# Performance work log

Measured on AMD Instinct MI355X. Metric: run time of the kernel, lower is better.

The kernel has to match this reference:

```python
import jax, jax.numpy as jnp
import numpy as np
import math

N_HEADS = 16
D_EMBED = 1024
D_CROSS = 768
FF_DIM = 4096
D_HEAD = D_EMBED // N_HEADS
LN_EPS = 1e-5


def layer_norm(h, g, b):
    mu = jnp.mean(h, axis=-1, keepdims=True)
    var = jnp.var(h, axis=-1, keepdims=True)
    return (h - mu) * jax.lax.rsqrt(var + LN_EPS) * g + b


def mha(q, k, v):
    # q: [B,Sq,D], k/v: [B,Skv,D] -> split heads, attend, merge
    B, Sq, _ = q.shape
    Skv = k.shape[1]
    qh = q.reshape(B, Sq, N_HEADS, D_HEAD).transpose(0, 2, 1, 3)
    kh = k.reshape(B, Skv, N_HEADS, D_HEAD).transpose(0, 2, 1, 3)
    vh = v.reshape(B, Skv, N_HEADS, D_HEAD).transpose(0, 2, 1, 3)
    scores = jnp.einsum('bhqd,bhkd->bhqk', qh, kh) / math.sqrt(D_HEAD)
    attn = jax.nn.softmax(scores, axis=-1)
    out = jnp.einsum('bhqk,bhkd->bhqd', attn, vh)
    return out.transpose(0, 2, 1, 3).reshape(B, Sq, D_EMBED)


def setup_inputs() -> dict:
    key = jax.random.key(0)
    ks = jax.random.split(key, 24)
    s = 0.02
    inp = {
        'x': jax.random.normal(ks[0], (4, 1024, D_EMBED), jnp.float32),
        'y': jax.random.normal(ks[1], (4, 77, D_CROSS), jnp.float32),
        # self-attention in_proj (d_embed -> 3*d_embed) and out_proj
        'w_qkv': jax.random.normal(ks[2], (D_EMBED, 3 * D_EMBED), jnp.float32) * s,
        'b_qkv': jnp.zeros((3 * D_EMBED,), jnp.float32),
        'w_so': jax.random.normal(ks[3], (D_EMBED, D_EMBED), jnp.float32) * s,
        'b_so': jnp.zeros((D_EMBED,), jnp.float32),
        # cross-attention projections
        'w_q': jax.random.normal(ks[4], (D_EMBED, D_EMBED), jnp.float32) * s,
        'b_q': jnp.zeros((D_EMBED,), jnp.float32),
        'w_k': jax.random.normal(ks[5], (D_CROSS, D_EMBED), jnp.float32) * s,
        'b_k': jnp.zeros((D_EMBED,), jnp.float32),
        'w_v': jax.random.normal(ks[6], (D_CROSS, D_EMBED), jnp.float32) * s,
        'b_v': jnp.zeros((D_EMBED,), jnp.float32),
        'w_co': jax.random.normal(ks[7], (D_EMBED, D_EMBED), jnp.float32) * s,
        'b_co': jnp.zeros((D_EMBED,), jnp.float32),
        # 3-layer FFN
        'w1': jax.random.normal(ks[8], (D_EMBED, FF_DIM), jnp.float32) * s,
        'b1': jnp.zeros((FF_DIM,), jnp.float32),
        'w2': jax.random.normal(ks[9], (FF_DIM, FF_DIM), jnp.float32) * s,
        'b2': jnp.zeros((FF_DIM,), jnp.float32),
        'w3': jax.random.normal(ks[10], (FF_DIM, D_EMBED), jnp.float32) * s,
        'b3': jnp.zeros((D_EMBED,), jnp.float32),
        # single shared LayerNorm (used 3 times, as in the torch module)
        'ln_g': jnp.ones((D_EMBED,), jnp.float32),
        'ln_b': jnp.zeros((D_EMBED,), jnp.float32),
    }
    return inp


def reference(x, y, w_qkv, b_qkv, w_so, b_so, w_q, b_q, w_k, b_k, w_v, b_v,
              w_co, b_co, w1, b1, w2, b2, w3, b3, ln_g, ln_b):
    # --- self attention (no causal mask) ---
    qkv = x @ w_qkv + b_qkv
    q, k, v = jnp.split(qkv, 3, axis=-1)
    sa = mha(q, k, v) @ w_so + b_so
    x = layer_norm(x + sa, ln_g, ln_b)
    # --- cross attention ---
    qc = x @ w_q + b_q
    kc = y @ w_k + b_k
    vc = y @ w_v + b_v
    ca = mha(qc, kc, vc) @ w_co + b_co
    x = layer_norm(x + ca, ln_g, ln_b)
    # --- 3-layer FFN with ReLU ---
    h = jax.nn.relu(x @ w1 + b1)
    h = jax.nn.relu(h @ w2 + b2)
    ff = h @ w3 + b3
    x = layer_norm(x + ff, ln_g, ln_b)
    return x
```

## Files before the change

kernel.cpp:

```cpp
#include <hip/hip_runtime.h>
#include <hip/hip_bf16.h>
#include <math.h>

typedef short v8s __attribute__((ext_vector_type(8)));
typedef float v4f __attribute__((ext_vector_type(4)));

__device__ __forceinline__ unsigned short f2bf(float f) {
  union { float f; unsigned u; } a; a.f = f;
  unsigned u = a.u + 0x7fffu + ((a.u >> 16) & 1u);
  return (unsigned short)(u >> 16);
}

__device__ __forceinline__ void gld_lds16(const unsigned short* g, unsigned short* l) {
  __builtin_amdgcn_global_load_lds(
      (const __attribute__((address_space(1))) void*)g,
      (__attribute__((address_space(3))) void*)l,
      16, 0, 0);
}

__global__ void cvt_f32_bf16(const float* __restrict__ in,
                             unsigned short* __restrict__ out, int n4) {
  int i = blockIdx.x * blockDim.x + threadIdx.x;
  if (i >= n4) return;
  float4 v = reinterpret_cast<const float4*>(in)[i];
  ushort4 o;
  o.x = f2bf(v.x); o.y = f2bf(v.y); o.z = f2bf(v.z); o.w = f2bf(v.w);
  reinterpret_cast<ushort4*>(out)[i] = o;
}

__global__ void cvt_transpose(const float* __restrict__ in,
                              unsigned short* __restrict__ out, int K, int N) {
  __shared__ float t[32][33];
  int bx = blockIdx.x, by = blockIdx.y;
  int tx = threadIdx.x, ty = threadIdx.y;
#pragma unroll
  for (int i = 0; i < 4; i++) {
    int k = by * 32 + ty + i * 8;
    t[ty + i * 8][tx] = in[(size_t)k * N + bx * 32 + tx];
  }
  __syncthreads();
#pragma unroll
  for (int i = 0; i < 4; i++) {
    int n = bx * 32 + ty + i * 8;
    out[(size_t)n * K + by * 32 + tx] = f2bf(t[tx][ty + i * 8]);
  }
}

template<bool RELU, bool OUTF, bool OUTB>
__global__ __launch_bounds__(256)
void gemm_bf16(const unsigned short* __restrict__ A,
               const unsigned short* __restrict__ BT,
               const float* __restrict__ bias,
               float* __restrict__ Cf, unsigned short* __restrict__ Cb,
               int M, int N, int K) {
  __shared__ __align__(16) unsigned short lA[128 * 64];
  __shared__ __align__(16) unsigned short lB[128 * 64];
  int tid  = threadIdx.x;
  int lane = tid & 63;
  int wave = tid >> 6;
  int wr = (wave >> 1) * 64;
  int wc = (wave & 1) * 64;
  int quad = lane >> 4;
  int l15  = lane & 15;
  int m0 = blockIdx.y * 128;
  int n0 = blockIdx.x * 128;

  int srow   = tid >> 3;
  int schunk = (tid & 7) ^ (srow & 7);
  const unsigned short* gA = A  + (size_t)(m0 + srow) * K + schunk * 8;
  const unsigned short* gB = BT + (size_t)(n0 + srow) * K + schunk * 8;
  unsigned short* ldsA = lA + wave * 512;
  unsigned short* ldsB = lB + wave * 512;
  const size_t rowblk = (size_t)32 * K;

  const v4f vzero = {0.f, 0.f, 0.f, 0.f};
  v4f acc[4][4];
#pragma unroll
  for (int i = 0; i < 4; i++)
#pragma unroll
    for (int j = 0; j < 4; j++) acc[i][j] = vzero;

  for (int k0 = 0; k0 < K; k0 += 64) {
#pragma unroll
    for (int i = 0; i < 4; i++) {
      gld_lds16(gA + k0 + i * rowblk, ldsA + i * 2048);
      gld_lds16(gB + k0 + i * rowblk, ldsB + i * 2048);
    }
    __syncthreads();
#pragma unroll
    for (int s = 0; s < 2; s++) {
      v8s aF[4], bF[4];
#pragma unroll
      for (int i = 0; i < 4; i++)
        aF[i] = *(const v8s*)&lA[(wr + i * 16 + l15) * 64 + (((s * 4 + quad) ^ (l15 & 7)) * 8)];
#pragma unroll
      for (int j = 0; j < 4; j++)
        bF[j] = *(const v8s*)&lB[(wc + j * 16 + l15) * 64 + (((s * 4 + quad) ^ (l15 & 7)) * 8)];
#pragma unroll
      for (int i = 0; i < 4; i++)
#pragma unroll
        for (int j = 0; j < 4; j++)
          acc[i][j] = __builtin_amdgcn_mfma_f32_16x16x32_bf16(aF[i], bF[j], acc[i][j], 0, 0, 0);
    }
    __syncthreads();
  }

#pragma unroll
  for (int j = 0; j < 4; j++) {
    int col = n0 + wc + j * 16 + l15;
    float bv = bias ? bias[col] : 0.f;
#pragma unroll
    for (int i = 0; i < 4; i++) {
#pragma unroll
      for (int r = 0; r < 4; r++) {
        int row = m0 + wr + i * 16 + quad * 4 + r;
        if (row < M) {
          float v = acc[i][j][r] + bv;
          if (RELU) v = fmaxf(v, 0.f);
          if (OUTF) Cf[(size_t)row * N + col] = v;
          if (OUTB) Cb[(size_t)row * N + col] = f2bf(v);
        }
      }
    }
  }
}

__global__ __launch_bounds__(256)
void attn_kernel(const unsigned short* __restrict__ Q,
                 const unsigned short* __restrict__ K,
                 const unsigned short* __restrict__ V,
                 unsigned short* __restrict__ O,
                 int q_rowstride, int kv_rowstride, int o_rowstride,
                 int q_batch_rows, int kv_batch_rows, int Skv, float scale) {
  __shared__ __align__(16) unsigned short lK[64][72];
  __shared__ __align__(16) unsigned short lV[64][72];
  __shared__ __align__(16) unsigned short lP[4][16][72];
  int tid  = threadIdx.x;
  int lane = tid & 63;
  int wave = tid >> 6;
  int quad = lane >> 4;
  int l15  = lane & 15;
  int qt = blockIdx.x, h = blockIdx.y, b = blockIdx.z;

  const unsigned short* Qb = Q + (size_t)b * q_batch_rows * q_rowstride + h * 64;
  const unsigned short* Kb = K + (size_t)b * kv_batch_rows * kv_rowstride + h * 64;
  const unsigned short* Vb = V + (size_t)b * kv_batch_rows * kv_rowstride + h * 64;

  v8s qf0, qf1;
  {
    const unsigned short* qr = Qb + (size_t)(qt * 64 + wave * 16 + l15) * q_rowstride + quad * 8;
    qf0 = *(const v8s*)(qr);
    qf1 = *(const v8s*)(qr + 32);
  }

  const v4f vzero = {0.f, 0.f, 0.f, 0.f};
  v4f o_acc[4];
#pragma unroll
  for (int t = 0; t < 4; t++) o_acc[t] = vzero;
  float m_r[4], l_r[4];
#pragma unroll
  for (int r = 0; r < 4; r++) { m_r[r] = -1e30f; l_r[r] = 0.f; }

  int sr = tid >> 2;
  int sc = (tid & 3) * 16;

  int nch = (Skv + 63) >> 6;
  for (int ch = 0; ch < nch; ch++) {
    int base = ch * 64;
    int gr = base + sr;
    v8s k0v = {}, k1v = {}, v0v = {}, v1v = {};
    if (gr < Skv) {
      const unsigned short* kp = Kb + (size_t)gr * kv_rowstride + sc;
      const unsigned short* vp = Vb + (size_t)gr * kv_rowstride + sc;
      k0v = *(const v8s*)kp;  k1v = *(const v8s*)(kp + 8);
      v0v = *(const v8s*)vp;  v1v = *(const v8s*)(vp + 8);
    }
    __syncthreads();
    *(v8s*)&lK[sr][sc]     = k0v;
    *(v8s*)&lK[sr][sc + 8] = k1v;
#pragma unroll
    for (int e = 0; e < 8; e++) {
      lV[sc + e][sr]     = (unsigned short)v0v[e];
      lV[sc + 8 + e][sr] = (unsigned short)v1v[e];
    }
    __syncthreads();

    float s[4][4];
#pragma unroll
    for (int t = 0; t < 4; t++) {
      v8s kf0 = *(const v8s*)&lK[t * 16 + l15][quad * 8];
      v8s kf1 = *(const v8s*)&lK[t * 16 + l15][32 + quad * 8];
      v4f sacc = vzero;
      sacc = __builtin_amdgcn_mfma_f32_16x16x32_bf16(qf0, kf0, sacc, 0, 0, 0);
      sacc = __builtin_amdgcn_mfma_f32_16x16x32_bf16(qf1, kf1, sacc, 0, 0, 0);
      int kvpos = base + t * 16 + l15;
      bool ok = kvpos < Skv;
#pragma unroll
      for (int r = 0; r < 4; r++) s[t][r] = ok ? sacc[r] * scale : -1e30f;
    }

#pragma unroll
    for (int r = 0; r < 4; r++) {
      float mx = fmaxf(fmaxf(s[0][r], s[1][r]), fmaxf(s[2][r], s[3][r]));
#pragma unroll
      for (int d = 1; d < 16; d <<= 1) mx = fmaxf(mx, __shfl_xor(mx, d));
      float mnew = fmaxf(m_r[r], mx);
      float alpha = __expf(m_r[r] - mnew);
      float sm = 0.f;
#pragma unroll
      for (int t = 0; t < 4; t++) { s[t][r] = __expf(s[t][r] - mnew); sm += s[t][r]; }
#pragma unroll
      for (int d = 1; d < 16; d <<= 1) sm += __shfl_xor(sm, d);
      l_r[r] = l_r[r] * alpha + sm;
      m_r[r] = mnew;
#pragma unroll
      for (int t = 0; t < 4; t++) o_acc[t][r] *= alpha;
    }

#pragma unroll
    for (int t = 0; t < 4; t++)
#pragma unroll
      for (int r = 0; r < 4; r++)
        lP[wave][quad * 4 + r][t * 16 + l15] = f2bf(s[t][r]);
    __syncthreads();
    v8s pf0 = *(const v8s*)&lP[wave][l15][quad * 8];
    v8s pf1 = *(const v8s*)&lP[wave][l15][32 + quad * 8];
#pragma unroll
    for (int t = 0; t < 4; t++) {
      v8s vf0 = *(const v8s*)&lV[t * 16 + l15][quad * 8];
      v8s vf1 = *(const v8s*)&lV[t * 16 + l15][32 + quad * 8];
      o_acc[t] = __builtin_amdgcn_mfma_f32_16x16x32_bf16(pf0, vf0, o_acc[t], 0, 0, 0);
      o_acc[t] = __builtin_amdgcn_mfma_f32_16x16x32_bf16(pf1, vf1, o_acc[t], 0, 0, 0);
    }
  }

  int orow0 = b * q_batch_rows + qt * 64 + wave * 16;
#pragma unroll
  for (int t = 0; t < 4; t++) {
#pragma unroll
    for (int r = 0; r < 4; r++) {
      float v = o_acc[t][r] / l_r[r];
      O[(size_t)(orow0 + quad * 4 + r) * o_rowstride + h * 64 + t * 16 + l15] = f2bf(v);
    }
  }
}

__global__ __launch_bounds__(256)
void ln_kernel(const float* base, const float* __restrict__ delta,
               const float* __restrict__ g, const float* __restrict__ bb,
               float* outf, unsigned short* __restrict__ outb) {
  __shared__ float red[8];
  int row = blockIdx.x;
  int tid = threadIdx.x;
  float4 vb = ((const float4*)(base  + (size_t)row * 1024))[tid];
  float4 vd = ((const float4*)(delta + (size_t)row * 1024))[tid];
  float v0 = vb.x + vd.x, v1 = vb.y + vd.y, v2 = vb.z + vd.z, v3 = vb.w + vd.w;
  float s = v0 + v1 + v2 + v3;
  float q = v0 * v0 + v1 * v1 + v2 * v2 + v3 * v3;
#pragma unroll
  for (int d = 1; d < 64; d <<= 1) { s += __shfl_xor(s, d); q += __shfl_xor(q, d); }
  int wave = tid >> 6, lane = tid & 63;
  if (lane == 0) { red[wave] = s; red[4 + wave] = q; }
  __syncthreads();
  s = red[0] + red[1] + red[2] + red[3];
  q = red[4] + red[5] + red[6] + red[7];
  float mean = s * (1.f / 1024.f);
  float var  = q * (1.f / 1024.f) - mean * mean;
  float rstd = rsqrtf(var + 1e-5f);
  float4 gg  = ((const float4*)g)[tid];
  float4 bv  = ((const float4*)bb)[tid];
  float o0 = (v0 - mean) * rstd * gg.x + bv.x;
  float o1 = (v1 - mean) * rstd * gg.y + bv.y;
  float o2 = (v2 - mean) * rstd * gg.z + bv.z;
  float o3 = (v3 - mean) * rstd * gg.w + bv.w;
  if (outf) {
    float4 o; o.x = o0; o.y = o1; o.z = o2; o.w = o3;
    ((float4*)(outf + (size_t)row * 1024))[tid] = o;
  }
  if (outb) {
    ushort4 u; u.x = f2bf(o0); u.y = f2bf(o1); u.z = f2bf(o2); u.w = f2bf(o3);
    ((ushort4*)(outb + (size_t)row * 1024))[tid] = u;
  }
}

extern "C" void kernel_launch(void* const* d_in, const int* in_sizes, int n_in,
                              void* d_out, int out_size, void* d_ws, size_t ws_size,
                              hipStream_t stream) {
  const float* x     = (const float*)d_in[0];
  const float* y     = (const float*)d_in[1];
  const float* w_qkv = (const float*)d_in[2];
  const float* b_qkv = (const float*)d_in[3];
  const float* w_so  = (const float*)d_in[4];
  const float* b_so  = (const float*)d_in[5];
  const float* w_q   = (const float*)d_in[6];
  const float* b_q   = (const float*)d_in[7];
  const float* w_k   = (const float*)d_in[8];
  const float* b_k   = (const float*)d_in[9];
  const float* w_v   = (const float*)d_in[10];
  const float* b_v   = (const float*)d_in[11];
  const float* w_co  = (const float*)d_in[12];
  const float* b_co  = (const float*)d_in[13];
  const float* w1    = (const float*)d_in[14];
  const float* b1    = (const float*)d_in[15];
  const float* w2    = (const float*)d_in[16];
  const float* b2    = (const float*)d_in[17];
  const float* w3    = (const float*)d_in[18];
  const float* b3    = (const float*)d_in[19];
  const float* ln_g  = (const float*)d_in[20];
  const float* ln_b  = (const float*)d_in[21];

  char* ws = (char*)d_ws;
  auto US = [&](size_t off) { return (unsigned short*)(ws + off); };
  auto FP = [&](size_t off) { return (float*)(ws + off); };

  constexpr size_t o_wqkv = 0;
  constexpr size_t o_wso  = o_wqkv + 3072ull * 1024 * 2;
  constexpr size_t o_wq   = o_wso  + 1024ull * 1024 * 2;
  constexpr size_t o_wk   = o_wq   + 1024ull * 1024 * 2;
  constexpr size_t o_wv   = o_wk   + 1024ull * 768 * 2;
  constexpr size_t o_wco  = o_wv   + 1024ull * 768 * 2;
  constexpr size_t o_w1   = o_wco  + 1024ull * 1024 * 2;
  constexpr size_t o_w2   = o_w1   + 4096ull * 1024 * 2;
  constexpr size_t o_w3   = o_w2   + 4096ull * 4096 * 2;
  constexpr size_t o_xf   = o_w3   + 1024ull * 4096 * 2;
  constexpr size_t o_xbf  = o_xf   + 4096ull * 1024 * 4;
  constexpr size_t o_ybf  = o_xbf  + 4096ull * 1024 * 2;
  constexpr size_t o_dlt  = o_ybf  + 308ull * 768 * 2;
  constexpr size_t o_R1   = o_dlt  + 4096ull * 1024 * 4;
  constexpr size_t o_attn = o_R1   + 4096ull * 3072 * 2;
  constexpr size_t o_R2   = o_attn + 4096ull * 1024 * 2;
  constexpr size_t o_qc = o_R1;
  constexpr size_t o_kc = o_R1 + 4096ull * 1024 * 2;
  constexpr size_t o_vc = o_kc + 308ull * 1024 * 2;
  constexpr size_t o_h1 = o_R1;
  constexpr size_t o_h2 = o_R2;

  dim3 tb(32, 8);
  cvt_transpose<<<dim3(96, 32),  tb, 0, stream>>>(w_qkv, US(o_wqkv), 1024, 3072);
  cvt_transpose<<<dim3(32, 32),  tb, 0, stream>>>(w_so,  US(o_wso),  1024, 1024);
  cvt_transpose<<<dim3(32, 32),  tb, 0, stream>>>(w_q,   US(o_wq),   1024, 1024);
  cvt_transpose<<<dim3(32, 24),  tb, 0, stream>>>(w_k,   US(o_wk),   768,  1024);
  cvt_transpose<<<dim3(32, 24),  tb, 0, stream>>>(w_v,   US(o_wv),   768,  1024);
  cvt_transpose<<<dim3(32, 32),  tb, 0, stream>>>(w_co,  US(o_wco),  1024, 1024);
  cvt_transpose<<<dim3(128, 32), tb, 0, stream>>>(w1,    US(o_w1),   1024, 4096);
  cvt_transpose<<<dim3(128, 128),tb, 0, stream>>>(w2,    US(o_w2),   4096, 4096);
  cvt_transpose<<<dim3(32, 128), tb, 0, stream>>>(w3,    US(o_w3),   4096, 1024);

  cvt_f32_bf16<<<4096, 256, 0, stream>>>(x, US(o_xbf), 4096 * 1024 / 4);
  cvt_f32_bf16<<<231, 256, 0, stream>>>(y, US(o_ybf), 4 * 77 * 768 / 4);

  gemm_bf16<false, false, true><<<dim3(24, 32), 256, 0, stream>>>(
      US(o_xbf), US(o_wqkv), b_qkv, nullptr, US(o_R1), 4096, 3072, 1024);
  attn_kernel<<<dim3(16, 16, 4), 256, 0, stream>>>(
      US(o_R1), US(o_R1) + 1024, US(o_R1) + 2048, US(o_attn),
      3072, 3072, 1024, 1024, 1024, 1024, 0.125f);
  gemm_bf16<false, true, false><<<dim3(8, 32), 256, 0, stream>>>(
      US(o_attn), US(o_wso), b_so, FP(o_dlt), nullptr, 4096, 1024, 1024);
  ln_kernel<<<4096, 256, 0, stream>>>(x, FP(o_dlt), ln_g, ln_b, FP(o_xf), US(o_xbf));

  gemm_bf16<false, false, true><<<dim3(8, 32), 256, 0, stream>>>(
      US(o_xbf), US(o_wq), b_q, nullptr, US(o_qc), 4096, 1024, 1024);
  gemm_bf16<false, false, true><<<dim3(8, 3), 256, 0, stream>>>(
      US(o_ybf), US(o_wk), b_k, nullptr, US(o_kc), 308, 1024, 768);
  gemm_bf16<false, false, true><<<dim3(8, 3), 256, 0, stream>>>(
      US(o_ybf), US(o_wv), b_v, nullptr, US(o_vc), 308, 1024, 768);
  attn_kernel<<<dim3(16, 16, 4), 256, 0, stream>>>(
      US(o_qc), US(o_kc), US(o_vc), US(o_attn),
      1024, 1024, 1024, 1024, 77, 77, 0.125f);
  gemm_bf16<false, true, false><<<dim3(8, 32), 256, 0, stream>>>(
      US(o_attn), US(o_wco), b_co, FP(o_dlt), nullptr, 4096, 1024, 1024);
  ln_kernel<<<4096, 256, 0, stream>>>(FP(o_xf), FP(o_dlt), ln_g, ln_b, FP(o_xf), US(o_xbf));

  gemm_bf16<true, false, true><<<dim3(32, 32), 256, 0, stream>>>(
      US(o_xbf), US(o_w1), b1, nullptr, US(o_h1), 4096, 4096, 1024);
  gemm_bf16<true, false, true><<<dim3(32, 32), 256, 0, stream>>>(
      US(o_h1), US(o_w2), b2, nullptr, US(o_h2), 4096, 4096, 4096);
  gemm_bf16<false, true, false><<<dim3(8, 32), 256, 0, stream>>>(
      US(o_h2), US(o_w3), b3, FP(o_dlt), nullptr, 4096, 1024, 4096);
  ln_kernel<<<4096, 256, 0, stream>>>(FP(o_xf), FP(o_dlt), ln_g, ln_b, (float*)d_out, nullptr);
}
```

Before: 837.5 us.

## Split-K the N=1024 projections, pre-transpose V, drop redundant attention barrier

The output projections and the final FFN GEMM (N=1024) now run as a two-way split-K over blockIdx.z. Each half writes its own fp32 partial buffer, and LayerNorm sums both deltas. This doubles the block count on GEMMs that otherwise fill only 256 tiles. A separate transpose_v kernel pre-lays V as [d][kv], so the attention kernel can do vector LDS stores instead of scalar transposed writes. A per-wave __syncthreads before reading P is also removed. The cost is an extra fp32 partial write and read, plus an extra small transpose kernel per attention.

Result: faster. 811.5 us (-3.1%).

```diff
diff --git a/kernel.cpp b/kernel.cpp
--- a/kernel.cpp
+++ b/kernel.cpp
@@ -3,6 +3,7 @@
 #include <math.h>
 
 typedef short v8s __attribute__((ext_vector_type(8)));
+typedef short v4s __attribute__((ext_vector_type(4)));
 typedef float v4f __attribute__((ext_vector_type(4)));
 
 __device__ __forceinline__ unsigned short f2bf(float f) {
@@ -46,13 +47,41 @@
   }
 }
 
+__global__ __launch_bounds__(256)
+void transpose_v(const unsigned short* __restrict__ V,
+                 unsigned short* __restrict__ Vt,
+                 int rowstride, int batch_rows, int Skv, int kvpad) {
+  __shared__ __align__(16) unsigned short t[64][80];
+  int ch = blockIdx.x, h = blockIdx.y, b = blockIdx.z;
+  int tid = threadIdx.x;
+  int sr = tid >> 2, sc = (tid & 3) * 16;
+  int gr = ch * 64 + sr;
+  v8s v0 = {}, v1 = {};
+  if (gr < Skv) {
+    const unsigned short* p = V + (size_t)(b * batch_rows + gr) * rowstride + h * 64 + sc;
+    v0 = *(const v8s*)p; v1 = *(const v8s*)(p + 8);
+  }
+  *(v8s*)&t[sr][sc]     = v0;
+  *(v8s*)&t[sr][sc + 8] = v1;
+  __syncthreads();
+  int d  = tid >> 2;
+  int k0 = (tid & 3) * 16;
+  unsigned short* o = Vt + ((size_t)(b * 16 + h) * 64 + d) * kvpad + ch * 64 + k0;
+  v8s o0, o1;
+#pragma unroll
+  for (int e = 0; e < 8; e++) { o0[e] = t[k0 + e][d]; o1[e] = t[k0 + 8 + e][d]; }
+  *(v8s*)o       = o0;
+  *(v8s*)(o + 8) = o1;
+}
+
 template<bool RELU, bool OUTF, bool OUTB>
 __global__ __launch_bounds__(256)
 void gemm_bf16(const unsigned short* __restrict__ A,
                const unsigned short* __restrict__ BT,
                const float* __restrict__ bias,
-               float* __restrict__ Cf, unsigned short* __restrict__ Cb,
-               int M, int N, int K) {
+               float* __restrict__ Cf, float* __restrict__ Cf2,
+               unsigned short* __restrict__ Cb,
+               int M, int N, int Kred, int ld) {
   __shared__ __align__(16) unsigned short lA[128 * 64];
   __shared__ __align__(16) unsigned short lB[128 * 64];
   int tid  = threadIdx.x;
@@ -64,14 +93,20 @@
   int l15  = lane & 15;
   int m0 = blockIdx.y * 128;
   int n0 = blockIdx.x * 128;
+  int z  = blockIdx.z;
+
+  const unsigned short* Az = A  + (size_t)z * Kred;
+  const unsigned short* Bz = BT + (size_t)z * Kred;
+  float* Cfo = z ? Cf2 : Cf;
+  const float* biasz = z ? nullptr : bias;
 
   int srow   = tid >> 3;
   int schunk = (tid & 7) ^ (srow & 7);
-  const unsigned short* gA = A  + (size_t)(m0 + srow) * K + schunk * 8;
-  const unsigned short* gB = BT + (size_t)(n0 + srow) * K + schunk * 8;
+  const unsigned short* gA = Az + (size_t)(m0 + srow) * ld + schunk * 8;
+  const unsigned short* gB = Bz + (size_t)(n0 + srow) * ld + schunk * 8;
   unsigned short* ldsA = lA + wave * 512;
   unsigned short* ldsB = lB + wave * 512;
-  const size_t rowblk = (size_t)32 * K;
+  const size_t rowblk = (size_t)32 * ld;
 
   const v4f vzero = {0.f, 0.f, 0.f, 0.f};
   v4f acc[4][4];
@@ -80,7 +115,7 @@
 #pragma unroll
     for (int j = 0; j < 4; j++) acc[i][j] = vzero;
 
-  for (int k0 = 0; k0 < K; k0 += 64) {
+  for (int k0 = 0; k0 < Kred; k0 += 64) {
 #pragma unroll
     for (int i = 0; i < 4; i++) {
       gld_lds16(gA + k0 + i * rowblk, ldsA + i * 2048);
@@ -108,7 +143,7 @@
 #pragma unroll
   for (int j = 0; j < 4; j++) {
     int col = n0 + wc + j * 16 + l15;
-    float bv = bias ? bias[col] : 0.f;
+    float bv = biasz ? biasz[col] : 0.f;
 #pragma unroll
     for (int i = 0; i < 4; i++) {
 #pragma unroll
@@ -117,8 +152,8 @@
         if (row < M) {
           float v = acc[i][j][r] + bv;
           if (RELU) v = fmaxf(v, 0.f);
-          if (OUTF) Cf[(size_t)row * N + col] = v;
-          if (OUTB) Cb[(size_t)row * N + col] = f2bf(v);
+          if (OUTF) Cfo[(size_t)row * N + col] = v;
+          if (OUTB && !z) Cb[(size_t)row * N + col] = f2bf(v);
         }
       }
     }
@@ -128,10 +163,11 @@
 __global__ __launch_bounds__(256)
 void attn_kernel(const unsigned short* __restrict__ Q,
                  const unsigned short* __restrict__ K,
-                 const unsigned short* __restrict__ V,
+                 const unsigned short* __restrict__ Vt,
                  unsigned short* __restrict__ O,
                  int q_rowstride, int kv_rowstride, int o_rowstride,
-                 int q_batch_rows, int kv_batch_rows, int Skv, float scale) {
+                 int q_batch_rows, int kv_batch_rows, int Skv, int kvpad,
+                 float scale) {
   __shared__ __align__(16) unsigned short lK[64][72];
   __shared__ __align__(16) unsigned short lV[64][72];
   __shared__ __align__(16) unsigned short lP[4][16][72];
@@ -142,9 +178,9 @@
   int l15  = lane & 15;
   int qt = blockIdx.x, h = blockIdx.y, b = blockIdx.z;
 
-  const unsigned short* Qb = Q + (size_t)b * q_batch_rows * q_rowstride + h * 64;
-  const unsigned short* Kb = K + (size_t)b * kv_batch_rows * kv_rowstride + h * 64;
-  const unsigned short* Vb = V + (size_t)b * kv_batch_rows * kv_rowstride + h * 64;
+  const unsigned short* Qb  = Q  + (size_t)b * q_batch_rows * q_rowstride + h * 64;
+  const unsigned short* Kb  = K  + (size_t)b * kv_batch_rows * kv_rowstride + h * 64;
+  const unsigned short* Vtb = Vt + ((size_t)(b * 16 + h) * 64) * kvpad;
 
   v8s qf0, qf1;
   {
@@ -168,20 +204,26 @@
   for (int ch = 0; ch < nch; ch++) {
     int base = ch * 64;
     int gr = base + sr;
-    v8s k0v = {}, k1v = {}, v0v = {}, v1v = {};
+    v8s k0v = {}, k1v = {};
     if (gr < Skv) {
       const unsigned short* kp = Kb + (size_t)gr * kv_rowstride + sc;
-      const unsigned short* vp = Vb + (size_t)gr * kv_rowstride + sc;
       k0v = *(const v8s*)kp;  k1v = *(const v8s*)(kp + 8);
-      v0v = *(const v8s*)vp;  v1v = *(const v8s*)(vp + 8);
-    }
+    }
+    const unsigned short* vp = Vtb + (size_t)sr * kvpad + base + sc;
+    v8s w0 = *(const v8s*)vp;
+    v8s w1 = *(const v8s*)(vp + 8);
     __syncthreads();
     *(v8s*)&lK[sr][sc]     = k0v;
     *(v8s*)&lK[sr][sc + 8] = k1v;
-#pragma unroll
-    for (int e = 0; e < 8; e++) {
-      lV[sc + e][sr]     = (unsigned short)v0v[e];
-      lV[sc + 8 + e][sr] = (unsigned short)v1v[e];
+    {
+      v4s a0 = {w0[0], w0[1], w0[2], w0[3]};
+      v4s a1 = {w0[4], w0[5], w0[6], w0[7]};
+      v4s a2 = {w1[0], w1[1], w1[2], w1[3]};
+      v4s a3 = {w1[4], w1[5], w1[6], w1[7]};
+      *(v4s*)&lV[sr][sc]      = a0;
+      *(v4s*)&lV[sr][sc + 4]  = a1;
+      *(v4s*)&lV[sr][sc + 8]  = a2;
+      *(v4s*)&lV[sr][sc + 12] = a3;
     }
     __syncthreads();
 
@@ -222,7 +264,6 @@
 #pragma unroll
       for (int r = 0; r < 4; r++)
         lP[wave][quad * 4 + r][t * 16 + l15] = f2bf(s[t][r]);
-    __syncthreads();
     v8s pf0 = *(const v8s*)&lP[wave][l15][quad * 8];
     v8s pf1 = *(const v8s*)&lP[wave][l15][32 + quad * 8];
 #pragma unroll
@@ -247,6 +288,7 @@
 
 __global__ __launch_bounds__(256)
 void ln_kernel(const float* base, const float* __restrict__ delta,
+               const float* __restrict__ delta2,
                const float* __restrict__ g, const float* __restrict__ bb,
                float* outf, unsigned short* __restrict__ outb) {
   __shared__ float red[8];
@@ -255,6 +297,10 @@
   float4 vb = ((const float4*)(base  + (size_t)row * 1024))[tid];
   float4 vd = ((const float4*)(delta + (size_t)row * 1024))[tid];
   float v0 = vb.x + vd.x, v1 = vb.y + vd.y, v2 = vb.z + vd.z, v3 = vb.w + vd.w;
+  if (delta2) {
+    float4 v2d = ((const float4*)(delta2 + (size_t)row * 1024))[tid];
+    v0 += v2d.x; v1 += v2d.y; v2 += v2d.z; v3 += v2d.w;
+  }
   float s = v0 + v1 + v2 + v3;
   float q = v0 * v0 + v1 * v1 + v2 * v2 + v3 * v3;
 #pragma unroll
@@ -329,11 +375,14 @@
   constexpr size_t o_R1   = o_dlt  + 4096ull * 1024 * 4;
   constexpr size_t o_attn = o_R1   + 4096ull * 3072 * 2;
   constexpr size_t o_R2   = o_attn + 4096ull * 1024 * 2;
-  constexpr size_t o_qc = o_R1;
-  constexpr size_t o_kc = o_R1 + 4096ull * 1024 * 2;
-  constexpr size_t o_vc = o_kc + 308ull * 1024 * 2;
-  constexpr size_t o_h1 = o_R1;
-  constexpr size_t o_h2 = o_R2;
+  constexpr size_t o_qc  = o_R1;
+  constexpr size_t o_kc  = o_R1 + 4096ull * 1024 * 2;
+  constexpr size_t o_vc  = o_kc + 308ull * 1024 * 2;
+  constexpr size_t o_h1  = o_R1;
+  constexpr size_t o_h2  = o_R2;
+  constexpr size_t o_dlt2 = o_R1;
+  constexpr size_t o_vtS = o_R2;
+  constexpr size_t o_vtC = o_R2 + 4ull * 16 * 64 * 1024 * 2;
 
   dim3 tb(32, 8);
   cvt_transpose<<<dim3(96, 32),  tb, 0, stream>>>(w_qkv, US(o_wqkv), 1024, 3072);
@@ -349,33 +398,40 @@
   cvt_f32_bf16<<<4096, 256, 0, stream>>>(x, US(o_xbf), 4096 * 1024 / 4);
   cvt_f32_bf16<<<231, 256, 0, stream>>>(y, US(o_ybf), 4 * 77 * 768 / 4);
 
-  gemm_bf16<false, false, true><<<dim3(24, 32), 256, 0, stream>>>(
-      US(o_xbf), US(o_wqkv), b_qkv, nullptr, US(o_R1), 4096, 3072, 1024);
+  gemm_bf16<false, false, true><<<dim3(24, 32, 1), 256, 0, stream>>>(
+      US(o_xbf), US(o_wqkv), b_qkv, nullptr, nullptr, US(o_R1), 4096, 3072, 1024, 1024);
+  transpose_v<<<dim3(16, 16, 4), 256, 0, stream>>>(
+      US(o_R1) + 2048, US(o_vtS), 3072, 1024, 1024, 1024);
   attn_kernel<<<dim3(16, 16, 4), 256, 0, stream>>>(
-      US(o_R1), US(o_R1) + 1024, US(o_R1) + 2048, US(o_attn),
-      3072, 3072, 1024, 1024, 1024, 1024, 0.125f);
-  gemm_bf16<false, true, false><<<dim3(8, 32), 256, 0, stream>>>(
-      US(o_attn), US(o_wso), b_so, FP(o_dlt), nullptr, 4096, 1024, 1024);
-  ln_kernel<<<4096, 256, 0, stream>>>(x, FP(o_dlt), ln_g, ln_b, FP(o_xf), US(o_xbf));
-
-  gemm_bf16<false, false, true><<<dim3(8, 32), 256, 0, stream>>>(
-      US(o_xbf), US(o_wq), b_q, nullptr, US(o_qc), 4096, 1024, 1024);
-  gemm_bf16<false, false, true><<<dim3(8, 3), 256, 0, stream>>>(
-      US(o_ybf), US(o_wk), b_k, nullptr, US(o_kc), 308, 1024, 768);
-  gemm_bf16<false, false, true><<<dim3(8, 3), 256, 0, stream>>>(
-      US(o_ybf), US(o_wv), b_v, nullptr, US(o_vc), 308, 1024, 768);
+      US(o_R1), US(o_R1) + 1024, US(o_vtS), US(o_attn),
+      3072, 3072, 1024, 1024, 1024, 1024, 1024, 0.125f);
+  gemm_bf16<false, true, false><<<dim3(8, 32, 2), 256, 0, stream>>>(
+      US(o_attn), US(o_wso), b_so, FP(o_dlt), FP(o_dlt2), nullptr, 4096, 1024, 512, 1024);
+  ln_kernel<<<4096, 256, 0, stream>>>(x, FP(o_dlt), FP(o_dlt2), ln_g, ln_b,
+                                      FP(o_xf), US(o_xbf));
+
+  gemm_bf16<false, false, true><<<dim3(8, 32, 1), 256, 0, stream>>>(
+      US(o_xbf), US(o_wq), b_q, nullptr, nullptr, US(o_qc), 4096, 1024, 1024, 1024);
+  gemm_bf16<false, false, true><<<dim3(8, 3, 1), 256, 0, stream>>>(
+      US(o_ybf), US(o_wk), b_k, nullptr, nullptr, US(o_kc), 308, 1024, 768, 768);
+  gemm_bf16<false, false, true><<<dim3(8, 3, 1), 256, 0, stream>>>(
+      US(o_ybf), US(o_wv), b_v, nullptr, nullptr, US(o_vc), 308, 1024, 768, 768);
+  transpose_v<<<dim3(2, 16, 4), 256, 0, stream>>>(
+      US(o_vc), US(o_vtC), 1024, 77, 77, 128);
   attn_kernel<<<dim3(16, 16, 4), 256, 0, stream>>>(
-      US(o_qc), US(o_kc), US(o_vc), US(o_attn),
-      1024, 1024, 1024, 1024, 77, 77, 0.125f);
-  gemm_bf16<false, true, false><<<dim3(8, 32), 256, 0, stream>>>(
-      US(o_attn), US(o_wco), b_co, FP(o_dlt), nullptr, 4096, 1024, 1024);
-  ln_kernel<<<4096, 256, 0, stream>>>(FP(o_xf), FP(o_dlt), ln_g, ln_b, FP(o_xf), US(o_xbf));
-
-  gemm_bf16<true, false, true><<<dim3(32, 32), 256, 0, stream>>>(
-      US(o_xbf), US(o_w1), b1, nullptr, US(o_h1), 4096, 4096, 1024);
-  gemm_bf16<true, false, true><<<dim3(32, 32), 256, 0, stream>>>(
-      US(o_h1), US(o_w2), b2, nullptr, US(o_h2), 4096, 4096, 4096);
-  gemm_bf16<false, true, false><<<dim3(8, 32), 256, 0, stream>>>(
-      US(o_h2), US(o_w3), b3, FP(o_dlt), nullptr, 4096, 1024, 4096);
-  ln_kernel<<<4096, 256, 0, stream>>>(FP(o_xf), FP(o_dlt), ln_g, ln_b, (float*)d_out, nullptr);
-}
+      US(o_qc), US(o_kc), US(o_vtC), US(o_attn),
+      1024, 1024, 1024, 1024, 77, 77, 128, 0.125f);
+  gemm_bf16<false, true, false><<<dim3(8, 32, 2), 256, 0, stream>>>(
+      US(o_attn), US(o_wco), b_co, FP(o_dlt), FP(o_dlt2), nullptr, 4096, 1024, 512, 1024);
+  ln_kernel<<<4096, 256, 0, stream>>>(FP(o_xf), FP(o_dlt), FP(o_dlt2), ln_g, ln_b,
+                                      FP(o_xf), US(o_xbf));
+
+  gemm_bf16<true, false, true><<<dim3(32, 32, 1), 256, 0, stream>>>(
+      US(o_xbf), US(o_w1), b1, nullptr, nullptr, US(o_h1), 4096, 4096, 1024, 1024);
+  gemm_bf16<true, false, true><<<dim3(32, 32, 1), 256, 0, stream>>>(
+      US(o_h1), US(o_w2), b2, nullptr, nullptr, US(o_h2), 4096, 4096, 4096, 4096);
+  gemm_bf16<false, true, false><<<dim3(8, 32, 2), 256, 0, stream>>>(
+      US(o_h2), US(o_w3), b3, FP(o_dlt), FP(o_dlt2), nullptr, 4096, 1024, 2048, 4096);
+  ln_kernel<<<4096, 256, 0, stream>>>(FP(o_xf), FP(o_dlt), FP(o_dlt2), ln_g, ln_b,
+                                      (float*)d_out, nullptr);
+}
```
